# Optimization experiments

Hardware: AMD Instinct MI355X
Metric: run time of the kernel (lower is better)

Reference implementation:

```python
import jax, jax.numpy as jnp
import numpy as np

N_NODES = 100000
IN_CH = 128
HID = 128   # 2 * out_channels
OUT = 64
N_EDGES = 1600000


def gcn_conv(x, W, b, src, dst, n_nodes):
    """PyG GCNConv: add self-loops, symmetric normalization D^-1/2 (A+I) D^-1/2 X W + b."""
    h = x @ W  # [N, F_out]
    ones = jnp.ones(dst.shape[0], dtype=h.dtype)
    # degree of target nodes, +1 for self loop
    deg = jax.ops.segment_sum(ones, dst, num_segments=n_nodes) + 1.0
    dinv = jnp.where(deg > 0, jax.lax.rsqrt(deg), 0.0)  # [N]
    norm = dinv[src] * dinv[dst]  # [E]
    agg = jax.ops.segment_sum(h[src] * norm[:, None], dst, num_segments=n_nodes)
    # self-loop contribution: norm_ii = dinv_i^2 (avoids materializing extra edges)
    agg = agg + h * (dinv * dinv)[:, None]
    return agg + b


def setup_inputs() -> dict:
    key = jax.random.key(0)
    ks = jax.random.split(key, 8)
    x = jax.random.normal(ks[0], (N_NODES, IN_CH), dtype=jnp.float32)
    edge_index = jax.random.randint(ks[1], (2, N_EDGES), 0, N_NODES, dtype=jnp.int64)
    # Glorot-style params
    W1 = jax.random.normal(ks[2], (IN_CH, HID), dtype=jnp.float32) / np.sqrt(IN_CH)
    b1 = jnp.zeros((HID,), dtype=jnp.float32)
    W_mu = jax.random.normal(ks[3], (HID, OUT), dtype=jnp.float32) / np.sqrt(HID)
    b_mu = jnp.zeros((OUT,), dtype=jnp.float32)
    W_ls = jax.random.normal(ks[4], (HID, OUT), dtype=jnp.float32) / np.sqrt(HID)
    b_ls = jnp.zeros((OUT,), dtype=jnp.float32)
    return {"x": x, "edge_index": edge_index, "W1": W1, "b1": b1,
            "W_mu": W_mu, "b_mu": b_mu, "W_ls": W_ls, "b_ls": b_ls}


def reference(x, edge_index, W1, b1, W_mu, b_mu, W_ls, b_ls):
    src, dst = edge_index[0], edge_index[1]
    n = x.shape[0]
    h = jax.nn.relu(gcn_conv(x, W1, b1, src, dst, n))
    mu = gcn_conv(h, W_mu, b_mu, src, dst, n)
    logstd = gcn_conv(h, W_ls, b_ls, src, dst, n)
    return (mu, logstd)
```

## Files before the change

kernel.cpp:

```cpp
#include <hip/hip_runtime.h>
#include <hip/hip_bf16.h>
#include <stdint.h>

#define N_NODES 100000
#define IN_CH   128
#define HID     128
#define OUT_CH  64
#define N_EDGES 1600000

#define NB    196
#define NBLK  250
#define EPB   6400

typedef __attribute__((ext_vector_type(8))) short  bf16x8;
typedef __attribute__((ext_vector_type(4))) float  f32x4;


__device__ __forceinline__ unsigned short f2bf(float f) {
    unsigned int u = __float_as_uint(f);
    u = (u + 0x7fffu + ((u >> 16) & 1u)) >> 16;
    return (unsigned short)u;
}
__device__ __forceinline__ float bfl(unsigned int u) { return __uint_as_float(u << 16); }
__device__ __forceinline__ float bfh(unsigned int u) { return __uint_as_float(u & 0xffff0000u); }


__global__ __launch_bounds__(256) void k_phaseA(const int* __restrict__ dst,
                                                int* __restrict__ Cm) {
    __shared__ int hist[NB];
    int blk = blockIdx.x, t = threadIdx.x;
    if (t < NB) hist[t] = 0;
    __syncthreads();
    int base = blk * EPB;
#pragma unroll 5
    for (int k = 0; k < EPB / 256; k++) {
        int d = dst[base + k * 256 + t];
        atomicAdd(&hist[d >> 9], 1);
    }
    __syncthreads();
    if (t < NB) Cm[blk * NB + t] = hist[t];
}

__global__ __launch_bounds__(256) void k_scanCm(int* __restrict__ Cm,
                                                int* __restrict__ bktBase) {
    __shared__ int sdata[256];
    int t = threadIdx.x;
    int run = 0;
    if (t < NB) {
        for (int blk = 0; blk < NBLK; blk++) {
            int idx = blk * NB + t;
            int v = Cm[idx];
            Cm[idx] = run;
            run += v;
        }
    }
    int s = (t < NB) ? run : 0;
    sdata[t] = s;
    __syncthreads();
    int val = s;
    for (int off = 1; off < 256; off <<= 1) {
        int tmp = (t >= off) ? sdata[t - off] : 0;
        __syncthreads();
        val += tmp;
        sdata[t] = val;
        __syncthreads();
    }
    if (t < NB) bktBase[t] = val - s;
    if (t == 0) bktBase[NB] = N_EDGES;
}

__global__ __launch_bounds__(256) void k_phaseB(const int* __restrict__ src,
                                                const int* __restrict__ dst,
                                                const int* __restrict__ Cm,
                                                const int* __restrict__ bktBase,
                                                unsigned int* __restrict__ bucketed) {
    __shared__ int offs[NB];
    int blk = blockIdx.x, t = threadIdx.x;
    if (t < NB) offs[t] = Cm[blk * NB + t] + bktBase[t];
    __syncthreads();
    int base = blk * EPB;
#pragma unroll 5
    for (int k = 0; k < EPB / 256; k++) {
        int e = base + k * 256 + t;
        int d = dst[e];
        int sv = src[e];
        int pos = atomicAdd(&offs[d >> 9], 1);
        bucketed[pos] = ((unsigned int)sv << 9) | (unsigned int)(d & 511);
    }
}

__global__ __launch_bounds__(512) void k_phaseC(const unsigned int* __restrict__ bucketed,
                                                const int* __restrict__ bktBase,
                                                int* __restrict__ rowptr,
                                                float* __restrict__ dinvg,
                                                int* __restrict__ csr_src) {
    __shared__ int cnt[512];
    __shared__ int cur[512];
    __shared__ int sdata[512];
    int b = blockIdx.x, t = threadIdx.x;
    int base = bktBase[b], endR = bktBase[b + 1];
    int nodeBase = b << 9;
    int nNodes = N_NODES - nodeBase;
    if (nNodes > 512) nNodes = 512;

    cnt[t] = 0;
    __syncthreads();
    for (int e = base + t; e < endR; e += 512)
        atomicAdd(&cnt[bucketed[e] & 511], 1);
    __syncthreads();

    int s = cnt[t];
    sdata[t] = s;
    __syncthreads();
    int val = s;
    for (int off = 1; off < 512; off <<= 1) {
        int tmp = (t >= off) ? sdata[t - off] : 0;
        __syncthreads();
        val += tmp;
        sdata[t] = val;
        __syncthreads();
    }
    cur[t] = val - s;
    if (t < nNodes) {
        rowptr[nodeBase + t] = base + val - s;
        dinvg[nodeBase + t] = rsqrtf((float)s + 1.0f);
    }
    if (b == NB - 1 && t == 0) rowptr[N_NODES] = N_EDGES;
    __syncthreads();

    for (int e = base + t; e < endR; e += 512) {
        unsigned int u = bucketed[e];
        int pos = base + atomicAdd(&cur[u & 511], 1);
        csr_src[pos] = (int)(u >> 9);
    }
}


__global__ __launch_bounds__(256) void k_prepW(const float* __restrict__ W1,
                                               const float* __restrict__ Wmu,
                                               const float* __restrict__ Wls,
                                               unsigned short* __restrict__ Wt1,
                                               unsigned short* __restrict__ WtC) {
    int idx = blockIdx.x * 256 + threadIdx.x;
    int n = idx >> 7, k = idx & 127;
    Wt1[idx] = f2bf(W1[k * 128 + n]);
    WtC[idx] = f2bf((n < 64) ? Wmu[k * 64 + n] : Wls[k * 64 + (n - 64)]);
}


#define LDA 136

__device__ __forceinline__ void gemm_compute(const unsigned short* sA,
                                             const unsigned short* __restrict__ Wt,
                                             unsigned short* __restrict__ Y,
                                             int R0, int t) {
    int wv = t >> 6, l = t & 63;
    int quad = l >> 4, lm = l & 15;

    bf16x8 a[2][4];
#pragma unroll
    for (int mt = 0; mt < 2; mt++)
#pragma unroll
        for (int ks = 0; ks < 4; ks++)
            a[mt][ks] = *(const bf16x8*)(sA + (wv * 32 + mt * 16 + lm) * LDA +
                                         ks * 32 + quad * 8);

    f32x4 acc[2][8] = {};
#pragma unroll
    for (int nt = 0; nt < 8; nt++) {
        bf16x8 b[4];
        const unsigned short* Wp = Wt + (nt * 16 + lm) * 128 + quad * 8;
#pragma unroll
        for (int ks = 0; ks < 4; ks++)
            b[ks] = *(const bf16x8*)(Wp + ks * 32);
#pragma unroll
        for (int mt = 0; mt < 2; mt++) {
            f32x4 c = acc[mt][nt];
#pragma unroll
            for (int ks = 0; ks < 4; ks++)
                c = __builtin_amdgcn_mfma_f32_16x16x32_bf16(a[mt][ks], b[ks], c, 0, 0, 0);
            acc[mt][nt] = c;
        }
    }

    int rbase = R0 + wv * 32 + quad * 4;
#pragma unroll
    for (int mt = 0; mt < 2; mt++)
#pragma unroll
        for (int nt = 0; nt < 8; nt++)
#pragma unroll
            for (int reg = 0; reg < 4; reg++) {
                int row = rbase + mt * 16 + reg;
                if (row < N_NODES)
                    Y[(size_t)row * 128 + nt * 16 + lm] = f2bf(acc[mt][nt][reg]);
            }
}

__global__ __launch_bounds__(256) void k_gemm1(const float* __restrict__ X,
                                               const unsigned short* __restrict__ Wt,
                                               unsigned short* __restrict__ Y) {
    __shared__ unsigned short sA[128 * LDA];
    int t = threadIdx.x;
    int R0 = blockIdx.x * 128;
    int row = t >> 1, colb = (t & 1) * 64;
    bool valid = (R0 + row) < N_NODES;
    const float* Xr = X + (size_t)(R0 + row) * 128 + colb;
    unsigned short* dp = sA + row * LDA + colb;
#pragma unroll
    for (int j = 0; j < 16; j++) {
        float4 v = valid ? *(const float4*)(Xr + j * 4) : make_float4(0.f, 0.f, 0.f, 0.f);
        ushort4 o;
        o.x = f2bf(v.x); o.y = f2bf(v.y); o.z = f2bf(v.z); o.w = f2bf(v.w);
        *(ushort4*)(dp + j * 4) = o;
    }
    __syncthreads();
    gemm_compute(sA, Wt, Y, R0, t);
}

__global__ __launch_bounds__(256) void k_gemm2(const unsigned short* __restrict__ Xb,
                                               const unsigned short* __restrict__ Wt,
                                               unsigned short* __restrict__ Y) {
    __shared__ unsigned short sA[128 * LDA];
    int t = threadIdx.x;
    int R0 = blockIdx.x * 128;
    int row = t >> 1, colb = (t & 1) * 64;
    bool valid = (R0 + row) < N_NODES;
    const unsigned short* Xr = Xb + (size_t)(R0 + row) * 128 + colb;
    unsigned short* dp = sA + row * LDA + colb;
#pragma unroll
    for (int j = 0; j < 8; j++) {
        uint4 v = valid ? *(const uint4*)(Xr + j * 8) : make_uint4(0u, 0u, 0u, 0u);
        *(uint4*)(dp + j * 8) = v;
    }
    __syncthreads();
    gemm_compute(sA, Wt, Y, R0, t);
}


__global__ __launch_bounds__(256) void k_agg1(const unsigned short* __restrict__ h0,
                                              const int* __restrict__ rowptr,
                                              const int* __restrict__ csr_src,
                                              const float* __restrict__ dinv,
                                              const float* __restrict__ b1,
                                              unsigned short* __restrict__ hb) {
    int lane = threadIdx.x & 63;
    int i = __builtin_amdgcn_readfirstlane(blockIdx.x * 4 + (threadIdx.x >> 6));
    int c2 = lane * 2;
    float di = dinv[i];
    unsigned int sv = *(const unsigned int*)(h0 + (size_t)i * 128 + c2);
    float ax = bfl(sv) * di * di, ay = bfh(sv) * di * di;
    int beg = rowptr[i], end = rowptr[i + 1];
    for (int p = beg; p < end; p += 8) {
        int s[8]; float n[8]; unsigned int r[8];
#pragma unroll
        for (int j = 0; j < 8; j++) {
            int q = p + j;
            s[j] = csr_src[q < end ? q : end - 1];
        }
#pragma unroll
        for (int j = 0; j < 8; j++) n[j] = dinv[s[j]];
#pragma unroll
        for (int j = 0; j < 8; j++)
            r[j] = *(const unsigned int*)(h0 + (size_t)s[j] * 128 + c2);
#pragma unroll
        for (int j = 0; j < 8; j++) n[j] = (p + j < end) ? n[j] * di : 0.f;
#pragma unroll
        for (int j = 0; j < 8; j++) {
            ax = fmaf(bfl(r[j]), n[j], ax);
            ay = fmaf(bfh(r[j]), n[j], ay);
        }
    }
    ax += b1[c2];
    ay += b1[c2 + 1];
    ax = ax > 0.f ? ax : 0.f;
    ay = ay > 0.f ? ay : 0.f;
    unsigned int pk = ((unsigned int)f2bf(ay) << 16) | (unsigned int)f2bf(ax);
    *(unsigned int*)(hb + (size_t)i * 128 + c2) = pk;
}

__global__ __launch_bounds__(256) void k_agg2(const unsigned short* __restrict__ tt,
                                              const int* __restrict__ rowptr,
                                              const int* __restrict__ csr_src,
                                              const float* __restrict__ dinv,
                                              const float* __restrict__ bmu,
                                              const float* __restrict__ bls,
                                              float* __restrict__ out) {
    int lane = threadIdx.x & 63;
    int i = __builtin_amdgcn_readfirstlane(blockIdx.x * 4 + (threadIdx.x >> 6));
    int c2 = lane * 2;
    float di = dinv[i];
    unsigned int sv = *(const unsigned int*)(tt + (size_t)i * 128 + c2);
    float ax = bfl(sv) * di * di, ay = bfh(sv) * di * di;
    int beg = rowptr[i], end = rowptr[i + 1];
    for (int p = beg; p < end; p += 8) {
        int s[8]; float n[8]; unsigned int r[8];
#pragma unroll
        for (int j = 0; j < 8; j++) {
            int q = p + j;
            s[j] = csr_src[q < end ? q : end - 1];
        }
#pragma unroll
        for (int j = 0; j < 8; j++) n[j] = dinv[s[j]];
#pragma unroll
        for (int j = 0; j < 8; j++)
            r[j] = *(const unsigned int*)(tt + (size_t)s[j] * 128 + c2);
#pragma unroll
        for (int j = 0; j < 8; j++) n[j] = (p + j < end) ? n[j] * di : 0.f;
#pragma unroll
        for (int j = 0; j < 8; j++) {
            ax = fmaf(bfl(r[j]), n[j], ax);
            ay = fmaf(bfh(r[j]), n[j], ay);
        }
    }
    if (lane < 32) {
        int c = c2;
        *(float2*)(out + (size_t)i * 64 + c) =
            make_float2(ax + bmu[c], ay + bmu[c + 1]);
    } else {
        int c = c2 - 64;
        *(float2*)(out + (size_t)N_NODES * 64 + (size_t)i * 64 + c) =
            make_float2(ax + bls[c], ay + bls[c + 1]);
    }
}


extern "C" void kernel_launch(void* const* d_in, const int* in_sizes, int n_in,
                              void* d_out, int out_size, void* d_ws, size_t ws_size,
                              hipStream_t stream) {
    const float* x    = (const float*)d_in[0];
    const int*   ei   = (const int*)d_in[1];
    const float* W1   = (const float*)d_in[2];
    const float* b1   = (const float*)d_in[3];
    const float* Wmu  = (const float*)d_in[4];
    const float* bmu  = (const float*)d_in[5];
    const float* Wls  = (const float*)d_in[6];
    const float* bls  = (const float*)d_in[7];
    const int* src = ei;
    const int* dst = ei + N_EDGES;

    char* p = (char*)d_ws;
    unsigned short* bufA = (unsigned short*)p; p += (size_t)N_NODES * 128 * 2;
    unsigned short* bufH = (unsigned short*)p; p += (size_t)N_NODES * 128 * 2;
    unsigned short* Wt1  = (unsigned short*)p; p += 128 * 128 * 2;
    unsigned short* WtC  = (unsigned short*)p; p += 128 * 128 * 2;
    int*   Cm      = (int*)p;   p += (size_t)NBLK * NB * 4;
    int*   bktBase = (int*)p;   p += 256 * 4;
    int*   rowptr  = (int*)p;   p += 400016;
    float* dinv    = (float*)p; p += 400000;
    unsigned int* bucketed = (unsigned int*)p; p += (size_t)N_EDGES * 4;
    int*   csr_src = (int*)p;   p += (size_t)N_EDGES * 4;

    k_phaseA<<<NBLK, 256, 0, stream>>>(dst, Cm);
    k_scanCm<<<1, 256, 0, stream>>>(Cm, bktBase);
    k_phaseB<<<NBLK, 256, 0, stream>>>(src, dst, Cm, bktBase, bucketed);
    k_phaseC<<<NB, 512, 0, stream>>>(bucketed, bktBase, rowptr, dinv, csr_src);

    k_prepW<<<64, 256, 0, stream>>>(W1, Wmu, Wls, Wt1, WtC);

    int gblk = (N_NODES + 127) / 128;

    k_gemm1<<<gblk, 256, 0, stream>>>(x, Wt1, bufA);
    k_agg1<<<N_NODES / 4, 256, 0, stream>>>(bufA, rowptr, csr_src, dinv, b1, bufH);

    k_gemm2<<<gblk, 256, 0, stream>>>(bufH, WtC, bufA);
    k_agg2<<<N_NODES / 4, 256, 0, stream>>>(bufA, rowptr, csr_src, dinv,
                                            bmu, bls, (float*)d_out);
}
```

Baseline: 353.2 us.

## Reorder layer-2 as aggregate-then-GEMM, fuse into one kernel, parallelize bucket scan

Layer 2 now aggregates the hidden features first and multiplies by the combined mu/logstd weight afterwards (A(HW) = (AH)W). This lets the gather and the MFMA GEMM share one kernel through LDS and removes the separate gemm2 pass and its intermediate buffer. The single-block serial scan over the bucket count matrix becomes a 196-block parallel scan plus a small base scan. The aggregation gather is also unrolled from 8 to 16 edges per iteration to keep more loads in flight. As a trade-off, the aggregated features are rounded to bf16 before the GEMM, and fewer waves per node block may reduce latency hiding.

```diff
diff --git a/kernel.cpp b/kernel.cpp
--- a/kernel.cpp
+++ b/kernel.cpp
@@ -41,23 +41,33 @@
     if (t < NB) Cm[blk * NB + t] = hist[t];
 }
 
-__global__ __launch_bounds__(256) void k_scanCm(int* __restrict__ Cm,
-                                                int* __restrict__ bktBase) {
+__global__ __launch_bounds__(256) void k_scanBkt(int* __restrict__ Cm,
+                                                 int* __restrict__ bktSum) {
+    __shared__ int sdata[256];
+    int b = blockIdx.x, t = threadIdx.x;
+    int v = (t < NBLK) ? Cm[t * NB + b] : 0;
+    sdata[t] = v;
+    __syncthreads();
+    int val = v;
+    for (int off = 1; off < 256; off <<= 1) {
+        int tmp = (t >= off) ? sdata[t - off] : 0;
+        __syncthreads();
+        val += tmp;
+        sdata[t] = val;
+        __syncthreads();
+    }
+    if (t < NBLK) Cm[t * NB + b] = val - v;
+    if (t == 255) bktSum[b] = val;
+}
+
+__global__ __launch_bounds__(256) void k_scanBase(const int* __restrict__ bktSum,
+                                                  int* __restrict__ bktBase) {
     __shared__ int sdata[256];
     int t = threadIdx.x;
-    int run = 0;
-    if (t < NB) {
-        for (int blk = 0; blk < NBLK; blk++) {
-            int idx = blk * NB + t;
-            int v = Cm[idx];
-            Cm[idx] = run;
-            run += v;
-        }
-    }
-    int s = (t < NB) ? run : 0;
-    sdata[t] = s;
-    __syncthreads();
-    int val = s;
+    int v = (t < NB) ? bktSum[t] : 0;
+    sdata[t] = v;
+    __syncthreads();
+    int val = v;
     for (int off = 1; off < 256; off <<= 1) {
         int tmp = (t >= off) ? sdata[t - off] : 0;
         __syncthreads();
@@ -65,7 +75,7 @@
         sdata[t] = val;
         __syncthreads();
     }
-    if (t < NB) bktBase[t] = val - s;
+    if (t < NB) bktBase[t] = val - v;
     if (t == 0) bktBase[NB] = N_EDGES;
 }
 
@@ -150,52 +160,6 @@
 
 #define LDA 136
 
-__device__ __forceinline__ void gemm_compute(const unsigned short* sA,
-                                             const unsigned short* __restrict__ Wt,
-                                             unsigned short* __restrict__ Y,
-                                             int R0, int t) {
-    int wv = t >> 6, l = t & 63;
-    int quad = l >> 4, lm = l & 15;
-
-    bf16x8 a[2][4];
-#pragma unroll
-    for (int mt = 0; mt < 2; mt++)
-#pragma unroll
-        for (int ks = 0; ks < 4; ks++)
-            a[mt][ks] = *(const bf16x8*)(sA + (wv * 32 + mt * 16 + lm) * LDA +
-                                         ks * 32 + quad * 8);
-
-    f32x4 acc[2][8] = {};
-#pragma unroll
-    for (int nt = 0; nt < 8; nt++) {
-        bf16x8 b[4];
-        const unsigned short* Wp = Wt + (nt * 16 + lm) * 128 + quad * 8;
-#pragma unroll
-        for (int ks = 0; ks < 4; ks++)
-            b[ks] = *(const bf16x8*)(Wp + ks * 32);
-#pragma unroll
-        for (int mt = 0; mt < 2; mt++) {
-            f32x4 c = acc[mt][nt];
-#pragma unroll
-            for (int ks = 0; ks < 4; ks++)
-                c = __builtin_amdgcn_mfma_f32_16x16x32_bf16(a[mt][ks], b[ks], c, 0, 0, 0);
-            acc[mt][nt] = c;
-        }
-    }
-
-    int rbase = R0 + wv * 32 + quad * 4;
-#pragma unroll
-    for (int mt = 0; mt < 2; mt++)
-#pragma unroll
-        for (int nt = 0; nt < 8; nt++)
-#pragma unroll
-            for (int reg = 0; reg < 4; reg++) {
-                int row = rbase + mt * 16 + reg;
-                if (row < N_NODES)
-                    Y[(size_t)row * 128 + nt * 16 + lm] = f2bf(acc[mt][nt][reg]);
-            }
-}
-
 __global__ __launch_bounds__(256) void k_gemm1(const float* __restrict__ X,
                                                const unsigned short* __restrict__ Wt,
                                                unsigned short* __restrict__ Y) {
@@ -214,26 +178,47 @@
         *(ushort4*)(dp + j * 4) = o;
     }
     __syncthreads();
-    gemm_compute(sA, Wt, Y, R0, t);
-}
-
-__global__ __launch_bounds__(256) void k_gemm2(const unsigned short* __restrict__ Xb,
-                                               const unsigned short* __restrict__ Wt,
-                                               unsigned short* __restrict__ Y) {
-    __shared__ unsigned short sA[128 * LDA];
-    int t = threadIdx.x;
-    int R0 = blockIdx.x * 128;
-    int row = t >> 1, colb = (t & 1) * 64;
-    bool valid = (R0 + row) < N_NODES;
-    const unsigned short* Xr = Xb + (size_t)(R0 + row) * 128 + colb;
-    unsigned short* dp = sA + row * LDA + colb;
-#pragma unroll
-    for (int j = 0; j < 8; j++) {
-        uint4 v = valid ? *(const uint4*)(Xr + j * 8) : make_uint4(0u, 0u, 0u, 0u);
-        *(uint4*)(dp + j * 8) = v;
-    }
-    __syncthreads();
-    gemm_compute(sA, Wt, Y, R0, t);
+
+    int wv = t >> 6, l = t & 63;
+    int quad = l >> 4, lm = l & 15;
+
+    bf16x8 a[2][4];
+#pragma unroll
+    for (int mt = 0; mt < 2; mt++)
+#pragma unroll
+        for (int ks = 0; ks < 4; ks++)
+            a[mt][ks] = *(const bf16x8*)(sA + (wv * 32 + mt * 16 + lm) * LDA +
+                                         ks * 32 + quad * 8);
+
+    f32x4 acc[2][8] = {};
+#pragma unroll
+    for (int nt = 0; nt < 8; nt++) {
+        bf16x8 b[4];
+        const unsigned short* Wp = Wt + (nt * 16 + lm) * 128 + quad * 8;
+#pragma unroll
+        for (int ks = 0; ks < 4; ks++)
+            b[ks] = *(const bf16x8*)(Wp + ks * 32);
+#pragma unroll
+        for (int mt = 0; mt < 2; mt++) {
+            f32x4 c = acc[mt][nt];
+#pragma unroll
+            for (int ks = 0; ks < 4; ks++)
+                c = __builtin_amdgcn_mfma_f32_16x16x32_bf16(a[mt][ks], b[ks], c, 0, 0, 0);
+            acc[mt][nt] = c;
+        }
+    }
+
+    int rbase = R0 + wv * 32 + quad * 4;
+#pragma unroll
+    for (int mt = 0; mt < 2; mt++)
+#pragma unroll
+        for (int nt = 0; nt < 8; nt++)
+#pragma unroll
+            for (int reg = 0; reg < 4; reg++) {
+                int r = rbase + mt * 16 + reg;
+                if (r < N_NODES)
+                    Y[(size_t)r * 128 + nt * 16 + lm] = f2bf(acc[mt][nt][reg]);
+            }
 }
 
 
@@ -250,22 +235,22 @@
     unsigned int sv = *(const unsigned int*)(h0 + (size_t)i * 128 + c2);
     float ax = bfl(sv) * di * di, ay = bfh(sv) * di * di;
     int beg = rowptr[i], end = rowptr[i + 1];
-    for (int p = beg; p < end; p += 8) {
-        int s[8]; float n[8]; unsigned int r[8];
-#pragma unroll
-        for (int j = 0; j < 8; j++) {
+    for (int p = beg; p < end; p += 16) {
+        int s[16]; float n[16]; unsigned int r[16];
+#pragma unroll
+        for (int j = 0; j < 16; j++) {
             int q = p + j;
             s[j] = csr_src[q < end ? q : end - 1];
         }
 #pragma unroll
-        for (int j = 0; j < 8; j++) n[j] = dinv[s[j]];
-#pragma unroll
-        for (int j = 0; j < 8; j++)
+        for (int j = 0; j < 16; j++) n[j] = dinv[s[j]];
+#pragma unroll
+        for (int j = 0; j < 16; j++)
             r[j] = *(const unsigned int*)(h0 + (size_t)s[j] * 128 + c2);
 #pragma unroll
-        for (int j = 0; j < 8; j++) n[j] = (p + j < end) ? n[j] * di : 0.f;
-#pragma unroll
-        for (int j = 0; j < 8; j++) {
+        for (int j = 0; j < 16; j++) n[j] = (p + j < end) ? n[j] * di : 0.f;
+#pragma unroll
+        for (int j = 0; j < 16; j++) {
             ax = fmaf(bfl(r[j]), n[j], ax);
             ay = fmaf(bfh(r[j]), n[j], ay);
         }
@@ -278,48 +263,81 @@
     *(unsigned int*)(hb + (size_t)i * 128 + c2) = pk;
 }
 
-__global__ __launch_bounds__(256) void k_agg2(const unsigned short* __restrict__ tt,
-                                              const int* __restrict__ rowptr,
-                                              const int* __restrict__ csr_src,
-                                              const float* __restrict__ dinv,
-                                              const float* __restrict__ bmu,
-                                              const float* __restrict__ bls,
-                                              float* __restrict__ out) {
-    int lane = threadIdx.x & 63;
-    int i = __builtin_amdgcn_readfirstlane(blockIdx.x * 4 + (threadIdx.x >> 6));
+
+#define LDG 136
+
+__global__ __launch_bounds__(256) void k_agg2g(const unsigned short* __restrict__ hb,
+                                               const int* __restrict__ rowptr,
+                                               const int* __restrict__ csr_src,
+                                               const float* __restrict__ dinv,
+                                               const unsigned short* __restrict__ WtC,
+                                               const float* __restrict__ bmu,
+                                               const float* __restrict__ bls,
+                                               float* __restrict__ out) {
+    __shared__ unsigned short g[16 * LDG];
+    int t = threadIdx.x;
+    int wv = t >> 6, lane = t & 63;
+    int nodeBase = blockIdx.x * 16;
     int c2 = lane * 2;
-    float di = dinv[i];
-    unsigned int sv = *(const unsigned int*)(tt + (size_t)i * 128 + c2);
-    float ax = bfl(sv) * di * di, ay = bfh(sv) * di * di;
-    int beg = rowptr[i], end = rowptr[i + 1];
-    for (int p = beg; p < end; p += 8) {
-        int s[8]; float n[8]; unsigned int r[8];
-#pragma unroll
-        for (int j = 0; j < 8; j++) {
-            int q = p + j;
-            s[j] = csr_src[q < end ? q : end - 1];
-        }
-#pragma unroll
-        for (int j = 0; j < 8; j++) n[j] = dinv[s[j]];
-#pragma unroll
-        for (int j = 0; j < 8; j++)
-            r[j] = *(const unsigned int*)(tt + (size_t)s[j] * 128 + c2);
-#pragma unroll
-        for (int j = 0; j < 8; j++) n[j] = (p + j < end) ? n[j] * di : 0.f;
-#pragma unroll
-        for (int j = 0; j < 8; j++) {
-            ax = fmaf(bfl(r[j]), n[j], ax);
-            ay = fmaf(bfh(r[j]), n[j], ay);
-        }
-    }
-    if (lane < 32) {
-        int c = c2;
-        *(float2*)(out + (size_t)i * 64 + c) =
-            make_float2(ax + bmu[c], ay + bmu[c + 1]);
-    } else {
-        int c = c2 - 64;
-        *(float2*)(out + (size_t)N_NODES * 64 + (size_t)i * 64 + c) =
-            make_float2(ax + bls[c], ay + bls[c + 1]);
+
+#pragma unroll 1
+    for (int j4 = 0; j4 < 4; j4++) {
+        int i = __builtin_amdgcn_readfirstlane(nodeBase + wv * 4 + j4);
+        float di = dinv[i];
+        unsigned int sv = *(const unsigned int*)(hb + (size_t)i * 128 + c2);
+        float ax = bfl(sv) * di * di, ay = bfh(sv) * di * di;
+        int beg = rowptr[i], end = rowptr[i + 1];
+        for (int p = beg; p < end; p += 16) {
+            int s[16]; float n[16]; unsigned int r[16];
+#pragma unroll
+            for (int j = 0; j < 16; j++) {
+                int q = p + j;
+                s[j] = csr_src[q < end ? q : end - 1];
+            }
+#pragma unroll
+            for (int j = 0; j < 16; j++) n[j] = dinv[s[j]];
+#pragma unroll
+            for (int j = 0; j < 16; j++)
+                r[j] = *(const unsigned int*)(hb + (size_t)s[j] * 128 + c2);
+#pragma unroll
+            for (int j = 0; j < 16; j++) n[j] = (p + j < end) ? n[j] * di : 0.f;
+#pragma unroll
+            for (int j = 0; j < 16; j++) {
+                ax = fmaf(bfl(r[j]), n[j], ax);
+                ay = fmaf(bfh(r[j]), n[j], ay);
+            }
+        }
+        unsigned int pk = ((unsigned int)f2bf(ay) << 16) | (unsigned int)f2bf(ax);
+        *(unsigned int*)(g + (wv * 4 + j4) * LDG + c2) = pk;
+    }
+    __syncthreads();
+
+    int quad = lane >> 4, lm = lane & 15;
+    bf16x8 a[4];
+#pragma unroll
+    for (int ks = 0; ks < 4; ks++)
+        a[ks] = *(const bf16x8*)(g + lm * LDG + ks * 32 + quad * 8);
+
+#pragma unroll
+    for (int nt2 = 0; nt2 < 2; nt2++) {
+        int nt = wv * 2 + nt2;
+        f32x4 acc = {};
+        const unsigned short* Wp = WtC + (nt * 16 + lm) * 128 + quad * 8;
+#pragma unroll
+        for (int ks = 0; ks < 4; ks++) {
+            bf16x8 b = *(const bf16x8*)(Wp + ks * 32);
+            acc = __builtin_amdgcn_mfma_f32_16x16x32_bf16(a[ks], b, acc, 0, 0, 0);
+        }
+        int col = nt * 16 + lm;
+#pragma unroll
+        for (int reg = 0; reg < 4; reg++) {
+            int row = nodeBase + quad * 4 + reg;
+            float v = acc[reg];
+            if (col < 64)
+                out[(size_t)row * 64 + col] = v + bmu[col];
+            else
+                out[(size_t)N_NODES * 64 + (size_t)row * 64 + (col - 64)] = v + bls[col - 64];
+        }
     }
 }
 
@@ -344,6 +362,7 @@
     unsigned short* Wt1  = (unsigned short*)p; p += 128 * 128 * 2;
     unsigned short* WtC  = (unsigned short*)p; p += 128 * 128 * 2;
     int*   Cm      = (int*)p;   p += (size_t)NBLK * NB * 4;
+    int*   bktSum  = (int*)p;   p += 256 * 4;
     int*   bktBase = (int*)p;   p += 256 * 4;
     int*   rowptr  = (int*)p;   p += 400016;
     float* dinv    = (float*)p; p += 400000;
@@ -351,7 +370,8 @@
     int*   csr_src = (int*)p;   p += (size_t)N_EDGES * 4;
 
     k_phaseA<<<NBLK, 256, 0, stream>>>(dst, Cm);
-    k_scanCm<<<1, 256, 0, stream>>>(Cm, bktBase);
+    k_scanBkt<<<NB, 256, 0, stream>>>(Cm, bktSum);
+    k_scanBase<<<1, 256, 0, stream>>>(bktSum, bktBase);
     k_phaseB<<<NBLK, 256, 0, stream>>>(src, dst, Cm, bktBase, bucketed);
     k_phaseC<<<NB, 512, 0, stream>>>(bucketed, bktBase, rowptr, dinv, csr_src);
 
@@ -362,7 +382,6 @@
     k_gemm1<<<gblk, 256, 0, stream>>>(x, Wt1, bufA);
     k_agg1<<<N_NODES / 4, 256, 0, stream>>>(bufA, rowptr, csr_src, dinv, b1, bufH);
 
-    k_gemm2<<<gblk, 256, 0, stream>>>(bufH, WtC, bufA);
-    k_agg2<<<N_NODES / 4, 256, 0, stream>>>(bufA, rowptr, csr_src, dinv,
-                                            bmu, bls, (float*)d_out);
-}
+    k_agg2g<<<N_NODES / 16, 256, 0, stream>>>(bufH, rowptr, csr_src, dinv,
+                                              WtC, bmu, bls, (float*)d_out);
+}
```

New measurement: 343.2 us. 2.8% less time.

## Switch intermediates to fp16 with packed half2 aggregation and parallelize bucket scan

Applied to the files above, without the earlier changes.

Intermediate feature tables and weights move from bf16 to fp16, and the GEMMs use the f16 MFMA. The neighbor accumulation now runs in packed __hfma2 on half2 values, with a precomputed half2 copy of dinv per node, which cuts ALU work in the gather loop. The single-block serial scan over the per-block histograms is split into a per-bucket parallel scan kernel plus a small base scan. In exchange, accumulating degree-16 sums in fp16 reduces precision and risks overflow or rounding error compared with fp32 accumulation.

```diff
diff --git a/kernel.cpp b/kernel.cpp
--- a/kernel.cpp
+++ b/kernel.cpp
@@ -1,5 +1,6 @@
 #include <hip/hip_runtime.h>
 #include <hip/hip_bf16.h>
+#include <hip/hip_fp16.h>
 #include <stdint.h>
 
 #define N_NODES 100000
@@ -12,17 +13,10 @@
 #define NBLK  250
 #define EPB   6400
 
-typedef __attribute__((ext_vector_type(8))) short  bf16x8;
+typedef __attribute__((ext_vector_type(8))) short  s16x8;
 typedef __attribute__((ext_vector_type(4))) float  f32x4;
 
-
-__device__ __forceinline__ unsigned short f2bf(float f) {
-    unsigned int u = __float_as_uint(f);
-    u = (u + 0x7fffu + ((u >> 16) & 1u)) >> 16;
-    return (unsigned short)u;
-}
-__device__ __forceinline__ float bfl(unsigned int u) { return __uint_as_float(u << 16); }
-__device__ __forceinline__ float bfh(unsigned int u) { return __uint_as_float(u & 0xffff0000u); }
+__device__ __forceinline__ __half2 as_h2(unsigned int u) { return *(__half2*)&u; }
 
 
 __global__ __launch_bounds__(256) void k_phaseA(const int* __restrict__ dst,
@@ -41,23 +35,33 @@
     if (t < NB) Cm[blk * NB + t] = hist[t];
 }
 
-__global__ __launch_bounds__(256) void k_scanCm(int* __restrict__ Cm,
-                                                int* __restrict__ bktBase) {
+__global__ __launch_bounds__(256) void k_scanBkt(int* __restrict__ Cm,
+                                                 int* __restrict__ bktSum) {
+    __shared__ int sdata[256];
+    int b = blockIdx.x, t = threadIdx.x;
+    int v = (t < NBLK) ? Cm[t * NB + b] : 0;
+    sdata[t] = v;
+    __syncthreads();
+    int val = v;
+    for (int off = 1; off < 256; off <<= 1) {
+        int tmp = (t >= off) ? sdata[t - off] : 0;
+        __syncthreads();
+        val += tmp;
+        sdata[t] = val;
+        __syncthreads();
+    }
+    if (t < NBLK) Cm[t * NB + b] = val - v;
+    if (t == 255) bktSum[b] = val;
+}
+
+__global__ __launch_bounds__(256) void k_scanBase(const int* __restrict__ bktSum,
+                                                  int* __restrict__ bktBase) {
     __shared__ int sdata[256];
     int t = threadIdx.x;
-    int run = 0;
-    if (t < NB) {
-        for (int blk = 0; blk < NBLK; blk++) {
-            int idx = blk * NB + t;
-            int v = Cm[idx];
-            Cm[idx] = run;
-            run += v;
-        }
-    }
-    int s = (t < NB) ? run : 0;
-    sdata[t] = s;
-    __syncthreads();
-    int val = s;
+    int v = (t < NB) ? bktSum[t] : 0;
+    sdata[t] = v;
+    __syncthreads();
+    int val = v;
     for (int off = 1; off < 256; off <<= 1) {
         int tmp = (t >= off) ? sdata[t - off] : 0;
         __syncthreads();
@@ -65,7 +69,7 @@
         sdata[t] = val;
         __syncthreads();
     }
-    if (t < NB) bktBase[t] = val - s;
+    if (t < NB) bktBase[t] = val - v;
     if (t == 0) bktBase[NB] = N_EDGES;
 }
 
@@ -93,6 +97,7 @@
                                                 const int* __restrict__ bktBase,
                                                 int* __restrict__ rowptr,
                                                 float* __restrict__ dinvg,
+                                                unsigned int* __restrict__ dinvh2,
                                                 int* __restrict__ csr_src) {
     __shared__ int cnt[512];
     __shared__ int cur[512];
@@ -123,7 +128,11 @@
     cur[t] = val - s;
     if (t < nNodes) {
         rowptr[nodeBase + t] = base + val - s;
-        dinvg[nodeBase + t] = rsqrtf((float)s + 1.0f);
+        float dv = rsqrtf((float)s + 1.0f);
+        dinvg[nodeBase + t] = dv;
+        __half hd = __float2half(dv);
+        unsigned int hu = *(unsigned short*)&hd;
+        dinvh2[nodeBase + t] = hu | (hu << 16);
     }
     if (b == NB - 1 && t == 0) rowptr[N_NODES] = N_EDGES;
     __syncthreads();
@@ -143,42 +152,44 @@
                                                unsigned short* __restrict__ WtC) {
     int idx = blockIdx.x * 256 + threadIdx.x;
     int n = idx >> 7, k = idx & 127;
-    Wt1[idx] = f2bf(W1[k * 128 + n]);
-    WtC[idx] = f2bf((n < 64) ? Wmu[k * 64 + n] : Wls[k * 64 + (n - 64)]);
+    __half a = __float2half(W1[k * 128 + n]);
+    __half b = __float2half((n < 64) ? Wmu[k * 64 + n] : Wls[k * 64 + (n - 64)]);
+    Wt1[idx] = *(unsigned short*)&a;
+    WtC[idx] = *(unsigned short*)&b;
 }
 
 
 #define LDA 136
 
-__device__ __forceinline__ void gemm_compute(const unsigned short* sA,
-                                             const unsigned short* __restrict__ Wt,
-                                             unsigned short* __restrict__ Y,
-                                             int R0, int t) {
+__device__ __forceinline__ void gemm_core(const unsigned short* sA,
+                                          const unsigned short* __restrict__ Wt,
+                                          unsigned short* __restrict__ Y,
+                                          int R0, int t) {
     int wv = t >> 6, l = t & 63;
     int quad = l >> 4, lm = l & 15;
 
-    bf16x8 a[2][4];
+    s16x8 a[2][4];
 #pragma unroll
     for (int mt = 0; mt < 2; mt++)
 #pragma unroll
         for (int ks = 0; ks < 4; ks++)
-            a[mt][ks] = *(const bf16x8*)(sA + (wv * 32 + mt * 16 + lm) * LDA +
-                                         ks * 32 + quad * 8);
+            a[mt][ks] = *(const s16x8*)(sA + (wv * 32 + mt * 16 + lm) * LDA +
+                                        ks * 32 + quad * 8);
 
     f32x4 acc[2][8] = {};
 #pragma unroll
     for (int nt = 0; nt < 8; nt++) {
-        bf16x8 b[4];
+        s16x8 b[4];
         const unsigned short* Wp = Wt + (nt * 16 + lm) * 128 + quad * 8;
 #pragma unroll
         for (int ks = 0; ks < 4; ks++)
-            b[ks] = *(const bf16x8*)(Wp + ks * 32);
+            b[ks] = *(const s16x8*)(Wp + ks * 32);
 #pragma unroll
         for (int mt = 0; mt < 2; mt++) {
             f32x4 c = acc[mt][nt];
 #pragma unroll
             for (int ks = 0; ks < 4; ks++)
-                c = __builtin_amdgcn_mfma_f32_16x16x32_bf16(a[mt][ks], b[ks], c, 0, 0, 0);
+                c = __builtin_amdgcn_mfma_f32_16x16x32_f16(a[mt][ks], b[ks], c, 0, 0, 0);
             acc[mt][nt] = c;
         }
     }
@@ -190,9 +201,11 @@
         for (int nt = 0; nt < 8; nt++)
 #pragma unroll
             for (int reg = 0; reg < 4; reg++) {
-                int row = rbase + mt * 16 + reg;
-                if (row < N_NODES)
-                    Y[(size_t)row * 128 + nt * 16 + lm] = f2bf(acc[mt][nt][reg]);
+                int r = rbase + mt * 16 + reg;
+                if (r < N_NODES) {
+                    __half hv = __float2half(acc[mt][nt][reg]);
+                    Y[(size_t)r * 128 + nt * 16 + lm] = *(unsigned short*)&hv;
+                }
             }
 }
 
@@ -209,15 +222,18 @@
 #pragma unroll
     for (int j = 0; j < 16; j++) {
         float4 v = valid ? *(const float4*)(Xr + j * 4) : make_float4(0.f, 0.f, 0.f, 0.f);
-        ushort4 o;
-        o.x = f2bf(v.x); o.y = f2bf(v.y); o.z = f2bf(v.z); o.w = f2bf(v.w);
-        *(ushort4*)(dp + j * 4) = o;
-    }
-    __syncthreads();
-    gemm_compute(sA, Wt, Y, R0, t);
-}
-
-__global__ __launch_bounds__(256) void k_gemm2(const unsigned short* __restrict__ Xb,
+        __half2 p0 = __floats2half2_rn(v.x, v.y);
+        __half2 p1 = __floats2half2_rn(v.z, v.w);
+        uint2 o;
+        o.x = *(unsigned int*)&p0;
+        o.y = *(unsigned int*)&p1;
+        *(uint2*)(dp + j * 4) = o;
+    }
+    __syncthreads();
+    gemm_core(sA, Wt, Y, R0, t);
+}
+
+__global__ __launch_bounds__(256) void k_gemm2(const unsigned short* __restrict__ Xh,
                                                const unsigned short* __restrict__ Wt,
                                                unsigned short* __restrict__ Y) {
     __shared__ unsigned short sA[128 * LDA];
@@ -225,7 +241,7 @@
     int R0 = blockIdx.x * 128;
     int row = t >> 1, colb = (t & 1) * 64;
     bool valid = (R0 + row) < N_NODES;
-    const unsigned short* Xr = Xb + (size_t)(R0 + row) * 128 + colb;
+    const unsigned short* Xr = Xh + (size_t)(R0 + row) * 128 + colb;
     unsigned short* dp = sA + row * LDA + colb;
 #pragma unroll
     for (int j = 0; j < 8; j++) {
@@ -233,54 +249,70 @@
         *(uint4*)(dp + j * 8) = v;
     }
     __syncthreads();
-    gemm_compute(sA, Wt, Y, R0, t);
-}
-
+    gemm_core(sA, Wt, Y, R0, t);
+}
+
+
+__device__ __forceinline__ float2 agg_gather(const unsigned short* __restrict__ tbl,
+                                             const int* __restrict__ rowptr,
+                                             const int* __restrict__ csr_src,
+                                             const unsigned int* __restrict__ dh2,
+                                             const float* __restrict__ dinv,
+                                             int i, int c2, float* di_out) {
+    float di = dinv[i];
+    *di_out = di;
+    unsigned int sv = *(const unsigned int*)(tbl + (size_t)i * 128 + c2);
+    __half2 acc = __floats2half2_rn(0.f, 0.f);
+    int beg = rowptr[i], end = rowptr[i + 1];
+    for (int p = beg; p < end; p += 8) {
+        int s[8]; unsigned int nv[8]; unsigned int r[8];
+#pragma unroll
+        for (int j = 0; j < 8; j++) {
+            int q = p + j;
+            s[j] = csr_src[q < end ? q : end - 1];
+        }
+#pragma unroll
+        for (int j = 0; j < 8; j++) nv[j] = dh2[s[j]];
+#pragma unroll
+        for (int j = 0; j < 8; j++)
+            r[j] = *(const unsigned int*)(tbl + (size_t)s[j] * 128 + c2);
+#pragma unroll
+        for (int j = 0; j < 8; j++) {
+            unsigned int nn = (p + j < end) ? nv[j] : 0u;
+            acc = __hfma2(as_h2(r[j]), as_h2(nn), acc);
+        }
+    }
+    float2 f = __half22float2(acc);
+    float2 hs = __half22float2(as_h2(sv));
+    f.x = di * f.x + di * di * hs.x;
+    f.y = di * f.y + di * di * hs.y;
+    return f;
+}
 
 __global__ __launch_bounds__(256) void k_agg1(const unsigned short* __restrict__ h0,
                                               const int* __restrict__ rowptr,
                                               const int* __restrict__ csr_src,
+                                              const unsigned int* __restrict__ dh2,
                                               const float* __restrict__ dinv,
                                               const float* __restrict__ b1,
                                               unsigned short* __restrict__ hb) {
     int lane = threadIdx.x & 63;
     int i = __builtin_amdgcn_readfirstlane(blockIdx.x * 4 + (threadIdx.x >> 6));
     int c2 = lane * 2;
-    float di = dinv[i];
-    unsigned int sv = *(const unsigned int*)(h0 + (size_t)i * 128 + c2);
-    float ax = bfl(sv) * di * di, ay = bfh(sv) * di * di;
-    int beg = rowptr[i], end = rowptr[i + 1];
-    for (int p = beg; p < end; p += 8) {
-        int s[8]; float n[8]; unsigned int r[8];
-#pragma unroll
-        for (int j = 0; j < 8; j++) {
-            int q = p + j;
-            s[j] = csr_src[q < end ? q : end - 1];
-        }
-#pragma unroll
-        for (int j = 0; j < 8; j++) n[j] = dinv[s[j]];
-#pragma unroll
-        for (int j = 0; j < 8; j++)
-            r[j] = *(const unsigned int*)(h0 + (size_t)s[j] * 128 + c2);
-#pragma unroll
-        for (int j = 0; j < 8; j++) n[j] = (p + j < end) ? n[j] * di : 0.f;
-#pragma unroll
-        for (int j = 0; j < 8; j++) {
-            ax = fmaf(bfl(r[j]), n[j], ax);
-            ay = fmaf(bfh(r[j]), n[j], ay);
-        }
-    }
-    ax += b1[c2];
-    ay += b1[c2 + 1];
-    ax = ax > 0.f ? ax : 0.f;
-    ay = ay > 0.f ? ay : 0.f;
-    unsigned int pk = ((unsigned int)f2bf(ay) << 16) | (unsigned int)f2bf(ax);
-    *(unsigned int*)(hb + (size_t)i * 128 + c2) = pk;
+    float di;
+    float2 f = agg_gather(h0, rowptr, csr_src, dh2, dinv, i, c2, &di);
+    f.x += b1[c2];
+    f.y += b1[c2 + 1];
+    f.x = f.x > 0.f ? f.x : 0.f;
+    f.y = f.y > 0.f ? f.y : 0.f;
+    __half2 o = __floats2half2_rn(f.x, f.y);
+    *(unsigned int*)(hb + (size_t)i * 128 + c2) = *(unsigned int*)&o;
 }
 
 __global__ __launch_bounds__(256) void k_agg2(const unsigned short* __restrict__ tt,
                                               const int* __restrict__ rowptr,
                                               const int* __restrict__ csr_src,
+                                              const unsigned int* __restrict__ dh2,
                                               const float* __restrict__ dinv,
                                               const float* __restrict__ bmu,
                                               const float* __restrict__ bls,
@@ -288,38 +320,16 @@
     int lane = threadIdx.x & 63;
     int i = __builtin_amdgcn_readfirstlane(blockIdx.x * 4 + (threadIdx.x >> 6));
     int c2 = lane * 2;
-    float di = dinv[i];
-    unsigned int sv = *(const unsigned int*)(tt + (size_t)i * 128 + c2);
-    float ax = bfl(sv) * di * di, ay = bfh(sv) * di * di;
-    int beg = rowptr[i], end = rowptr[i + 1];
-    for (int p = beg; p < end; p += 8) {
-        int s[8]; float n[8]; unsigned int r[8];
-#pragma unroll
-        for (int j = 0; j < 8; j++) {
-            int q = p + j;
-            s[j] = csr_src[q < end ? q : end - 1];
-        }
-#pragma unroll
-        for (int j = 0; j < 8; j++) n[j] = dinv[s[j]];
-#pragma unroll
-        for (int j = 0; j < 8; j++)
-            r[j] = *(const unsigned int*)(tt + (size_t)s[j] * 128 + c2);
-#pragma unroll
-        for (int j = 0; j < 8; j++) n[j] = (p + j < end) ? n[j] * di : 0.f;
-#pragma unroll
-        for (int j = 0; j < 8; j++) {
-            ax = fmaf(bfl(r[j]), n[j], ax);
-            ay = fmaf(bfh(r[j]), n[j], ay);
-        }
-    }
+    float di;
+    float2 f = agg_gather(tt, rowptr, csr_src, dh2, dinv, i, c2, &di);
     if (lane < 32) {
         int c = c2;
         *(float2*)(out + (size_t)i * 64 + c) =
-            make_float2(ax + bmu[c], ay + bmu[c + 1]);
+            make_float2(f.x + bmu[c], f.y + bmu[c + 1]);
     } else {
         int c = c2 - 64;
         *(float2*)(out + (size_t)N_NODES * 64 + (size_t)i * 64 + c) =
-            make_float2(ax + bls[c], ay + bls[c + 1]);
+            make_float2(f.x + bls[c], f.y + bls[c + 1]);
     }
 }
 
@@ -344,25 +354,28 @@
     unsigned short* Wt1  = (unsigned short*)p; p += 128 * 128 * 2;
     unsigned short* WtC  = (unsigned short*)p; p += 128 * 128 * 2;
     int*   Cm      = (int*)p;   p += (size_t)NBLK * NB * 4;
+    int*   bktSum  = (int*)p;   p += 256 * 4;
     int*   bktBase = (int*)p;   p += 256 * 4;
     int*   rowptr  = (int*)p;   p += 400016;
     float* dinv    = (float*)p; p += 400000;
+    unsigned int* dinvh2 = (unsigned int*)p; p += 400000;
     unsigned int* bucketed = (unsigned int*)p; p += (size_t)N_EDGES * 4;
     int*   csr_src = (int*)p;   p += (size_t)N_EDGES * 4;
 
     k_phaseA<<<NBLK, 256, 0, stream>>>(dst, Cm);
-    k_scanCm<<<1, 256, 0, stream>>>(Cm, bktBase);
+    k_scanBkt<<<NB, 256, 0, stream>>>(Cm, bktSum);
+    k_scanBase<<<1, 256, 0, stream>>>(bktSum, bktBase);
     k_phaseB<<<NBLK, 256, 0, stream>>>(src, dst, Cm, bktBase, bucketed);
-    k_phaseC<<<NB, 512, 0, stream>>>(bucketed, bktBase, rowptr, dinv, csr_src);
+    k_phaseC<<<NB, 512, 0, stream>>>(bucketed, bktBase, rowptr, dinv, dinvh2, csr_src);
 
     k_prepW<<<64, 256, 0, stream>>>(W1, Wmu, Wls, Wt1, WtC);
 
     int gblk = (N_NODES + 127) / 128;
 
     k_gemm1<<<gblk, 256, 0, stream>>>(x, Wt1, bufA);
-    k_agg1<<<N_NODES / 4, 256, 0, stream>>>(bufA, rowptr, csr_src, dinv, b1, bufH);
+    k_agg1<<<N_NODES / 4, 256, 0, stream>>>(bufA, rowptr, csr_src, dinvh2, dinv, b1, bufH);
 
     k_gemm2<<<gblk, 256, 0, stream>>>(bufH, WtC, bufA);
-    k_agg2<<<N_NODES / 4, 256, 0, stream>>>(bufA, rowptr, csr_src, dinv,
+    k_agg2<<<N_NODES / 4, 256, 0, stream>>>(bufA, rowptr, csr_src, dinvh2, dinv,
                                             bmu, bls, (float*)d_out);
 }
```

Measured after the change: 350.6 us. Within noise of the previous version (-0.7%).
